# Kernel optimization log

Hardware: AMD Instinct MI355X
Metric: run time of the kernel (lower is better)

The kernel has to match this reference:

```python
import jax, jax.numpy as jnp
import numpy as np

CAP = 6.0
EPS = 1e-5

def _layernorm(x, g, b):
    mu = jnp.mean(x, axis=-1, keepdims=True)
    var = jnp.mean(jnp.square(x - mu), axis=-1, keepdims=True)
    return (x - mu) * jax.lax.rsqrt(var + EPS) * g + b

def setup_inputs() -> dict:
    key = jax.random.key(0)
    B, S, D, H = 4, 1024, 1024, 16
    DF = int(D * 2.0)
    ks = jax.random.split(key, 8)
    inp = {
        "x": jax.random.normal(ks[0], (B, S, D), dtype=jnp.float32),
        "mask": jnp.tril(jnp.ones((S, S), dtype=bool)),  # causal block mask
        "qkv_w": jax.random.normal(ks[1], (3 * D, D), dtype=jnp.float32) * 0.02,
        "qkv_b": jnp.zeros((3 * D,), dtype=jnp.float32),
        "out_w": jax.random.normal(ks[2], (D, D), dtype=jnp.float32) * 0.02,
        "out_b": jnp.zeros((D,), dtype=jnp.float32),
        "ln1_g": jnp.ones((D,), dtype=jnp.float32),
        "ln1_b": jnp.zeros((D,), dtype=jnp.float32),
        "ln2_g": jnp.ones((D,), dtype=jnp.float32),
        "ln2_b": jnp.zeros((D,), dtype=jnp.float32),
        "ff1_w": jax.random.normal(ks[3], (DF, D), dtype=jnp.float32) * 0.02,
        "ff1_b": jnp.zeros((DF,), dtype=jnp.float32),
        "ff2_w": jax.random.normal(ks[4], (D, DF), dtype=jnp.float32) * 0.02,
        "ff2_b": jnp.zeros((D,), dtype=jnp.float32),
    }
    return inp

def reference(x, mask, qkv_w, qkv_b, out_w, out_b, ln1_g, ln1_b, ln2_g, ln2_b,
              ff1_w, ff1_b, ff2_w, ff2_b):
    B, S, D = x.shape
    H = 16
    dh = D // H
    res = x
    h = _layernorm(x, ln1_g, ln1_b)
    qkv = h @ qkv_w.T + qkv_b                       # [B,S,3D]
    qkv = qkv.reshape(B, S, 3, H, dh).transpose(2, 0, 3, 1, 4)  # [3,B,H,S,dh]
    q, k, v = qkv[0], qkv[1], qkv[2]
    scores = jnp.einsum('bhqd,bhkd->bhqk', q, k) / jnp.sqrt(jnp.float32(dh))
    scores = CAP * jnp.tanh(scores / CAP)            # logit soft-cap score_mod
    scores = jnp.where(mask, scores, jnp.float32(-1e9))
    attn = jax.nn.softmax(scores, axis=-1)
    o = jnp.einsum('bhqk,bhkd->bhqd', attn, v)       # [B,H,S,dh]
    o = o.transpose(0, 2, 1, 3).reshape(B, S, D)
    x = res + (o @ out_w.T + out_b)
    h2 = _layernorm(x, ln2_g, ln2_b)
    ff = jax.nn.gelu(h2 @ ff1_w.T + ff1_b, approximate=False) @ ff2_w.T + ff2_b
    return x + ff
```

## Files before the change

kernel.cpp:

```cpp
#include <hip/hip_runtime.h>
#include <hip/hip_bf16.h>
#include <cmath>

#define NROWS 4096
#define DM    1024

typedef unsigned short u16;
typedef __attribute__((ext_vector_type(8))) short short8;
typedef __attribute__((ext_vector_type(4))) float floatx4;

#if __has_builtin(__builtin_amdgcn_exp2f)
#define EXP2F(x) __builtin_amdgcn_exp2f(x)
#else
#define EXP2F(x) exp2f(x)
#endif
#if __has_builtin(__builtin_amdgcn_rcpf)
#define RCPF(x) __builtin_amdgcn_rcpf(x)
#else
#define RCPF(x) (1.0f / (x))
#endif

__device__ __forceinline__ u16 f2bf(float f) {
    unsigned int u = __float_as_uint(f);
    return (u16)((u + 0x7fffu + ((u >> 16) & 1u)) >> 16);
}

__device__ __forceinline__ size_t pk_off(int row, int k, int KB) {
    const int rt = row >> 6, i = (row >> 4) & 3, lr = row & 15;
    const int kb = k >> 6, s = (k >> 5) & 1, lq = (k >> 3) & 3, j = k & 7;
    return ((((size_t)(rt * KB + kb) * 2 + s) * 4 + i) * 64 + lq * 16 + lr) * 8 + j;
}

__global__ __launch_bounds__(256) void castln_kernel(
    const float* __restrict__ s0, const float* __restrict__ s1,
    const float* __restrict__ s2, const float* __restrict__ s3,
    u16* __restrict__ d0, u16* __restrict__ d1,
    u16* __restrict__ d2, u16* __restrict__ d3,
    const float* __restrict__ x, const float* __restrict__ g,
    const float* __restrict__ beta, u16* __restrict__ hout)
{
    const int bid = blockIdx.x;
    if (bid < 8192) {
        const float* s; u16* d; int base, kbits, KB;
        if (bid < 3072)      { s = s0; d = d0; base = bid;        kbits = 10; KB = 16; }
        else if (bid < 4096) { s = s1; d = d1; base = bid - 3072; kbits = 10; KB = 16; }
        else if (bid < 6144) { s = s2; d = d2; base = bid - 4096; kbits = 10; KB = 16; }
        else                 { s = s3; d = d3; base = bid - 6144; kbits = 11; KB = 32; }
        const int idx = (base * 256 + threadIdx.x) * 4;
        const float4 v = *(const float4*)(s + idx);
        const int row = idx >> kbits, k = idx & ((1 << kbits) - 1);
        *(ushort4*)(d + pk_off(row, k, KB)) =
            make_ushort4(f2bf(v.x), f2bf(v.y), f2bf(v.z), f2bf(v.w));
        return;
    }
    const int row = bid - 8192;
    const int t = threadIdx.x;
    const float4 v = ((const float4*)(x + (size_t)row * DM))[t];
    float s = v.x + v.y + v.z + v.w;
    #pragma unroll
    for (int off = 32; off > 0; off >>= 1) s += __shfl_xor(s, off);
    __shared__ float red[4];
    const int wid = t >> 6;
    if ((t & 63) == 0) red[wid] = s;
    __syncthreads();
    const float mean = (red[0] + red[1] + red[2] + red[3]) * (1.0f / DM);
    const float dx = v.x - mean, dy = v.y - mean, dz = v.z - mean, dw = v.w - mean;
    float ss = dx*dx + dy*dy + dz*dz + dw*dw;
    #pragma unroll
    for (int off = 32; off > 0; off >>= 1) ss += __shfl_xor(ss, off);
    __syncthreads();
    if ((t & 63) == 0) red[wid] = ss;
    __syncthreads();
    const float var = (red[0] + red[1] + red[2] + red[3]) * (1.0f / DM);
    const float rstd = rsqrtf(var + 1e-5f);
    const float4 gv = ((const float4*)g)[t];
    const float4 bv = ((const float4*)beta)[t];
    *(ushort4*)(hout + pk_off(row, t * 4, 16)) = make_ushort4(
        f2bf(dx * rstd * gv.x + bv.x), f2bf(dy * rstd * gv.y + bv.y),
        f2bf(dz * rstd * gv.z + bv.z), f2bf(dw * rstd * gv.w + bv.w));
}

__global__ __launch_bounds__(256) void ln_kernel(
    const float* __restrict__ x, const float* __restrict__ g,
    const float* __restrict__ beta, u16* __restrict__ out)
{
    const int row = blockIdx.x;
    const int t = threadIdx.x;
    const float4 v = ((const float4*)(x + (size_t)row * DM))[t];
    float s = v.x + v.y + v.z + v.w;
    #pragma unroll
    for (int off = 32; off > 0; off >>= 1) s += __shfl_xor(s, off);
    __shared__ float red[4];
    const int wid = t >> 6;
    if ((t & 63) == 0) red[wid] = s;
    __syncthreads();
    const float mean = (red[0] + red[1] + red[2] + red[3]) * (1.0f / DM);
    const float dx = v.x - mean, dy = v.y - mean, dz = v.z - mean, dw = v.w - mean;
    float ss = dx*dx + dy*dy + dz*dz + dw*dw;
    #pragma unroll
    for (int off = 32; off > 0; off >>= 1) ss += __shfl_xor(ss, off);
    __syncthreads();
    if ((t & 63) == 0) red[wid] = ss;
    __syncthreads();
    const float var = (red[0] + red[1] + red[2] + red[3]) * (1.0f / DM);
    const float rstd = rsqrtf(var + 1e-5f);
    const float4 gv = ((const float4*)g)[t];
    const float4 bv = ((const float4*)beta)[t];
    *(ushort4*)(out + pk_off(row, t * 4, 16)) = make_ushort4(
        f2bf(dx * rstd * gv.x + bv.x), f2bf(dy * rstd * gv.y + bv.y),
        f2bf(dz * rstd * gv.z + bv.z), f2bf(dw * rstd * gv.w + bv.w));
}

__device__ __forceinline__ float gelu_f(float v) {
    return 0.5f * v * (1.0f + erff(v * 0.70710678118654752f));
}

template <int ACT, int OUTMODE, int TM>
__global__ __launch_bounds__(256, TM == 128 ? 3 : 4) void gemm_pk_kernel(
    const u16* __restrict__ A, const u16* __restrict__ W,
    const float* __restrict__ bias, const float* __restrict__ res,
    void* __restrict__ Cout, u16* __restrict__ vpout, u16* __restrict__ kpout,
    int N, int K)
{
    constexpr int MI = TM / 32;
    constexpr int SMEMB = (OUTMODE == 1) ? 34816 : 17408;
    __shared__ __align__(16) char smem[SMEMB];
    float* Cs = (float*)smem;

    const int tid = threadIdx.x;
    const int w = tid >> 6, l = tid & 63;
    const int lr = l & 15, lq = l >> 4;
    const int wm = w >> 1, wn = w & 1;

    const int fid = blockIdx.x;
    const int NB = (N >> 7) >> 3;
    const int xcd = fid & 7;
    const int kk = fid >> 3;
    constexpr int MT_BITS = (TM == 128) ? 5 : 6;
    constexpr int MT_MASK = (1 << MT_BITS) - 1;
    const int nt = xcd * NB + (kk >> MT_BITS);
    const int mt = kk & MT_MASK;
    const int m0 = mt * TM, n0 = nt * 128;
    const int KB = K >> 6;

    const int art = (TM == 128) ? (mt * 2 + wm) : mt;
    const u16* Ab = A + (size_t)art * KB * 4096 + l * 8;
    const u16* Wb = W + (size_t)(nt * 2 + wn) * KB * 4096 + l * 8;

    floatx4 acc[MI][4] = {};
    short8 a0[MI], b0[4], a1[MI], b1[4];
    #pragma unroll
    for (int i = 0; i < MI; i++) {
        const int fi = (TM == 128) ? i : (wm * 2 + i);
        a0[i] = *(const short8*)(Ab + fi * 512);
    }
    #pragma unroll
    for (int j = 0; j < 4; j++) b0[j] = *(const short8*)(Wb + j * 512);

    const int steps = K >> 5;
    for (int t = 0; t < steps; t += 2) {
        const u16* An = Ab + (size_t)(t + 1) * 2048;
        const u16* Wn = Wb + (size_t)(t + 1) * 2048;
        #pragma unroll
        for (int i = 0; i < MI; i++) {
            const int fi = (TM == 128) ? i : (wm * 2 + i);
            a1[i] = *(const short8*)(An + fi * 512);
        }
        #pragma unroll
        for (int j = 0; j < 4; j++) b1[j] = *(const short8*)(Wn + j * 512);
        #pragma unroll
        for (int i = 0; i < MI; i++)
            #pragma unroll
            for (int j = 0; j < 4; j++)
                acc[i][j] = __builtin_amdgcn_mfma_f32_16x16x32_bf16(a0[i], b0[j], acc[i][j], 0, 0, 0);
        if (t + 2 < steps) {
            const u16* An2 = Ab + (size_t)(t + 2) * 2048;
            const u16* Wn2 = Wb + (size_t)(t + 2) * 2048;
            #pragma unroll
            for (int i = 0; i < MI; i++) {
                const int fi = (TM == 128) ? i : (wm * 2 + i);
                a0[i] = *(const short8*)(An2 + fi * 512);
            }
            #pragma unroll
            for (int j = 0; j < 4; j++) b0[j] = *(const short8*)(Wn2 + j * 512);
        }
        #pragma unroll
        for (int i = 0; i < MI; i++)
            #pragma unroll
            for (int j = 0; j < 4; j++)
                acc[i][j] = __builtin_amdgcn_mfma_f32_16x16x32_bf16(a1[i], b1[j], acc[i][j], 0, 0, 0);
    }

    if (OUTMODE == 1) {
        short* Ts = (short*)smem;
        float bj[4];
        #pragma unroll
        for (int j = 0; j < 4; j++) bj[j] = bias[n0 + wn * 64 + j * 16 + lr];
        const bool isV = (n0 >= 2048);
        if (isV) {
            #pragma unroll
            for (int i = 0; i < 4; i++)
                #pragma unroll
                for (int j = 0; j < 4; j++) {
                    const int vcol_l = wn * 64 + j * 16 + lr;
                    const int sbase = wm * 64 + i * 16 + lq * 4;
                    #pragma unroll
                    for (int rp = 0; rp < 2; rp++) {
                        const unsigned pkv =
                            (unsigned)f2bf(acc[i][j][rp * 2] + bj[j]) |
                            ((unsigned)f2bf(acc[i][j][rp * 2 + 1] + bj[j]) << 16);
                        *(unsigned*)&Ts[vcol_l * 136 + sbase + rp * 2] = pkv;
                    }
                }
        } else {
            #pragma unroll
            for (int i = 0; i < 4; i++)
                #pragma unroll
                for (int j = 0; j < 4; j++)
                    #pragma unroll
                    for (int r = 0; r < 4; r++) {
                        const int row_l = wm * 64 + i * 16 + lq * 4 + r;
                        const int col_l = wn * 64 + j * 16 + lr;
                        Ts[row_l * 136 + col_l] = (short)f2bf(acc[i][j][r] + bj[j]);
                    }
        }
        __syncthreads();
        u16* dbuf = isV ? vpout : (n0 >= 1024 ? kpout : (u16*)Cout);
        const int hbase = (n0 & 1023) >> 6;
        const int l0 = (tid * 2) & 63, subp = tid >> 6, sp = (tid >> 5) & 1;
        #pragma unroll
        for (int tl = 0; tl < 2; tl++) {
            const int mg = m0 + tl * 64;
            const int bb2 = mg >> 10, ktile = (mg & 1023) >> 6;
            #pragma unroll
            for (int hl = 0; hl < 2; hl++) {
                const int hh = hbase + hl;
                u16* dst = dbuf + ((size_t)(bb2 * 16 + hh) * 16 + ktile) * 4096 + tid * 16;
                #pragma unroll
                for (int half = 0; half < 2; half++) {
                    const int ll = l0 + half;
                    short8 seg;
                    if (isV) {
                        const int vcol_l = hl * 64 + subp * 16 + (ll & 15);
                        const int srow = tl * 64 + sp * 32 + ((ll >> 4) & 3) * 8;
                        seg = *(const short8*)&Ts[vcol_l * 136 + srow];
                    } else {
                        const int row_l = tl * 64 + subp * 16 + (ll & 15);
                        const int col_l = hl * 64 + sp * 32 + ((ll >> 4) & 3) * 8;
                        seg = *(const short8*)&Ts[row_l * 136 + col_l];
                    }
                    *(short8*)(dst + half * 8) = seg;
                }
            }
        }
        return;
    }

    #pragma unroll
    for (int i = 0; i < MI; i++) {
        __syncthreads();
        #pragma unroll
        for (int r = 0; r < 4; r++) {
            const int rl = wm * 16 + lq * 4 + r;
            #pragma unroll
            for (int j = 0; j < 4; j++)
                Cs[rl * 136 + wn * 64 + j * 16 + lr] = acc[i][j][r];
        }
        __syncthreads();
        #pragma unroll
        for (int q = 0; q < 2; q++) {
            const int s2 = tid * 2 + q;
            const int rid = s2 >> 4, c8 = s2 & 15;
            const int rr = m0 + (rid >> 4) * (TM / 2) + i * 16 + (rid & 15);
            const int col = c8 * 8;
            float vv[8];
            const float4 v0 = *(const float4*)&Cs[rid * 136 + col];
            const float4 v1 = *(const float4*)&Cs[rid * 136 + col + 4];
            const float4 ba = *(const float4*)&bias[n0 + col];
            const float4 bb4 = *(const float4*)&bias[n0 + col + 4];
            vv[0] = v0.x + ba.x;  vv[1] = v0.y + ba.y;  vv[2] = v0.z + ba.z;  vv[3] = v0.w + ba.w;
            vv[4] = v1.x + bb4.x; vv[5] = v1.y + bb4.y; vv[6] = v1.z + bb4.z; vv[7] = v1.w + bb4.w;
            if (ACT) {
                #pragma unroll
                for (int e = 0; e < 8; e++) vv[e] = gelu_f(vv[e]);
            }
            if (OUTMODE == 0) {
                const size_t o0 = (size_t)rr * N + n0 + col;
                if (res) {
                    const float4 r0 = *(const float4*)&res[o0];
                    const float4 r1 = *(const float4*)&res[o0 + 4];
                    vv[0]+=r0.x; vv[1]+=r0.y; vv[2]+=r0.z; vv[3]+=r0.w;
                    vv[4]+=r1.x; vv[5]+=r1.y; vv[6]+=r1.z; vv[7]+=r1.w;
                }
                *(float4*)((float*)Cout + o0)     = make_float4(vv[0], vv[1], vv[2], vv[3]);
                *(float4*)((float*)Cout + o0 + 4) = make_float4(vv[4], vv[5], vv[6], vv[7]);
            } else {
                short8 ov;
                #pragma unroll
                for (int e = 0; e < 8; e++) ov[e] = (short)f2bf(vv[e]);
                *(short8*)((u16*)Cout + pk_off(rr, n0 + col, N >> 6)) = ov;
            }
        }
    }
}

__global__ __launch_bounds__(256, 3) void attn_mfma_kernel(
    const u16* __restrict__ qp, const u16* __restrict__ kp,
    const u16* __restrict__ vp, u16* __restrict__ o)
{
    __shared__ __align__(16) short Ps[4][1152];
    __shared__ __align__(16) short Os[4096];

    const int qt = 15 - blockIdx.y;
    const int bh = blockIdx.x;
    const int b = bh >> 4, h = bh & 15;
    const int tid = threadIdx.x;
    const int w = tid >> 6, l = tid & 63;
    const int C = l & 15, Qd = l >> 4;

    const float C1f = 0.0601122935f, C2f = -17.3123404907f;

    const size_t headoff = (size_t)(b * 16 + h) * 16 * 4096;
    const u16* qb = qp + headoff + (size_t)qt * 4096 + w * 1024 + l * 8;
    const u16* kb = kp + headoff + l * 8;
    const u16* vb = vp + headoff + l * 8;

    short8 qf[2];
    qf[0] = *(const short8*)qb;
    qf[1] = *(const short8*)(qb + 512);

    float l_i = 0.f;
    floatx4 oacc[4] = {};

    short8 kf[8];
    #pragma unroll
    for (int i = 0; i < 8; i++) kf[i] = *(const short8*)(kb + i * 512);

    for (int kt = 0; kt <= qt; kt++) {
        const u16* vv_ = vb + (size_t)kt * 4096;
        short8 vf[8];
        #pragma unroll
        for (int j = 0; j < 8; j++) vf[j] = *(const short8*)(vv_ + j * 512);

        floatx4 sacc[4] = {};
        #pragma unroll
        for (int mt = 0; mt < 4; mt++)
            #pragma unroll
            for (int s = 0; s < 2; s++)
                sacc[mt] = __builtin_amdgcn_mfma_f32_16x16x32_bf16(kf[mt * 2 + s], qf[s], sacc[mt], 0, 0, 0);

        if (kt < qt) {
            const u16* kn_ = kb + (size_t)(kt + 1) * 4096;
            #pragma unroll
            for (int i = 0; i < 8; i++) kf[i] = *(const short8*)(kn_ + i * 512);
        }

        float p[16];
        float rs = 0.f;
        const bool diag = (kt == qt);
        const int qrow = qt * 64 + w * 16 + C;
        #pragma unroll
        for (int mt = 0; mt < 4; mt++)
            #pragma unroll
            for (int r = 0; r < 4; r++) {
                const float e = EXP2F(sacc[mt][r] * C1f);
                float pv = EXP2F(C2f * RCPF(e + 1.0f));
                if (diag) {
                    const int krow = kt * 64 + mt * 16 + Qd * 4 + r;
                    if (krow > qrow) pv = 0.f;
                }
                p[mt * 4 + r] = pv;
                rs += pv;
            }
        rs += __shfl_xor(rs, 16);
        rs += __shfl_xor(rs, 32);
        l_i += rs;

        #pragma unroll
        for (int mt = 0; mt < 4; mt++)
            #pragma unroll
            for (int pr = 0; pr < 2; pr++) {
                union { __hip_bfloat162 b2; unsigned u; } cv;
                cv.b2 = __float22bfloat162_rn(
                    make_float2(p[mt * 4 + pr * 2], p[mt * 4 + pr * 2 + 1]));
                *(unsigned*)&Ps[w][C * 72 + mt * 16 + Qd * 4 + pr * 2] = cv.u;
            }
        short8 pf[2];
        pf[0] = *(const short8*)&Ps[w][C * 72 + Qd * 8];
        pf[1] = *(const short8*)&Ps[w][C * 72 + 32 + Qd * 8];

        #pragma unroll
        for (int dt = 0; dt < 4; dt++)
            #pragma unroll
            for (int s = 0; s < 2; s++)
                oacc[dt] = __builtin_amdgcn_mfma_f32_16x16x32_bf16(pf[s], vf[dt * 2 + s], oacc[dt], 0, 0, 0);
    }

    float linv[4];
    #pragma unroll
    for (int r = 0; r < 4; r++) linv[r] = RCPF(__shfl(l_i, Qd * 4 + r));
    #pragma unroll
    for (int dt = 0; dt < 4; dt++) {
        const int s = dt >> 1;
        const int lqp = (dt & 1) * 2 + (C >> 3);
        const int jj = C & 7;
        #pragma unroll
        for (int r = 0; r < 4; r++)
            Os[((s * 4 + w) * 64 + lqp * 16 + Qd * 4 + r) * 8 + jj] =
                (short)f2bf(oacc[dt][r] * linv[r]);
    }
    __syncthreads();
    u16* obase = o + (size_t)((b * 16 + qt) * 16 + h) * 4096 + tid * 16;
    *(short8*)obase       = *(const short8*)&Os[tid * 16];
    *(short8*)(obase + 8) = *(const short8*)&Os[tid * 16 + 8];
}

extern "C" void kernel_launch(void* const* d_in, const int* in_sizes, int n_in,
                              void* d_out, int out_size, void* d_ws, size_t ws_size,
                              hipStream_t stream)
{
    (void)in_sizes; (void)n_in; (void)out_size; (void)ws_size;
    const float* x     = (const float*)d_in[0];
    const float* qkv_w = (const float*)d_in[2];
    const float* qkv_b = (const float*)d_in[3];
    const float* out_w = (const float*)d_in[4];
    const float* out_b = (const float*)d_in[5];
    const float* ln1_g = (const float*)d_in[6];
    const float* ln1_b = (const float*)d_in[7];
    const float* ln2_g = (const float*)d_in[8];
    const float* ln2_b = (const float*)d_in[9];
    const float* ff1_w = (const float*)d_in[10];
    const float* ff1_b = (const float*)d_in[11];
    const float* ff2_w = (const float*)d_in[12];
    const float* ff2_b = (const float*)d_in[13];
    float* out = (float*)d_out;

    u16* qpbuf = (u16*)d_ws;
    u16* kpbuf = qpbuf + 4194304;
    u16* vpbuf = kpbuf + 4194304;
    u16* hbuf  = (u16*)((char*)d_ws + 33554432);
    u16* obuf  = (u16*)((char*)d_ws + 41943040);
    u16* wq    = (u16*)((char*)d_ws + 50331648);
    u16* wo = wq + 3145728;
    u16* w1 = wo + 1048576;
    u16* w2 = w1 + 2097152;
    u16* ff1buf = (u16*)d_ws;

    castln_kernel<<<12288, 256, 0, stream>>>(
        qkv_w, out_w, ff1_w, ff2_w, wq, wo, w1, w2, x, ln1_g, ln1_b, hbuf);
    gemm_pk_kernel<0,1,128><<<768, 256, 0, stream>>>(
        hbuf, wq, qkv_b, nullptr, qpbuf, vpbuf, kpbuf, 3072, 1024);
    attn_mfma_kernel<<<dim3(64, 16), 256, 0, stream>>>(qpbuf, kpbuf, vpbuf, obuf);
    gemm_pk_kernel<0,0,64><<<512, 256, 0, stream>>>(
        obuf, wo, out_b, x, out, nullptr, nullptr, 1024, 1024);
    ln_kernel<<<NROWS, 256, 0, stream>>>(out, ln2_g, ln2_b, hbuf);
    gemm_pk_kernel<1,2,128><<<512, 256, 0, stream>>>(
        hbuf, w1, ff1_b, nullptr, ff1buf, nullptr, nullptr, 2048, 1024);
    gemm_pk_kernel<0,0,64><<<512, 256, 0, stream>>>(
        ff1buf, w2, ff2_b, out, out, nullptr, nullptr, 1024, 2048);
}
```

Measured before the change: 295.2 us.

## Stage GEMM operand tiles through LDS with async global_load_lds double buffering

```diff
diff --git a/kernel.cpp b/kernel.cpp
--- a/kernel.cpp
+++ b/kernel.cpp
@@ -23,6 +23,12 @@
 __device__ __forceinline__ u16 f2bf(float f) {
     unsigned int u = __float_as_uint(f);
     return (u16)((u + 0x7fffu + ((u >> 16) & 1u)) >> 16);
+}
+
+__device__ __forceinline__ void gl_lds16(const u16* g, u16* l) {
+    __builtin_amdgcn_global_load_lds(
+        (const __attribute__((address_space(1))) unsigned int*)g,
+        (__attribute__((address_space(3))) unsigned int*)l, 16, 0, 0);
 }
 
 __device__ __forceinline__ size_t pk_off(int row, int k, int KB) {
@@ -116,15 +122,18 @@
 }
 
 template <int ACT, int OUTMODE, int TM>
-__global__ __launch_bounds__(256, TM == 128 ? 3 : 4) void gemm_pk_kernel(
+__global__ __launch_bounds__(256, 2) void gemm_pk_kernel(
     const u16* __restrict__ A, const u16* __restrict__ W,
     const float* __restrict__ bias, const float* __restrict__ res,
     void* __restrict__ Cout, u16* __restrict__ vpout, u16* __restrict__ kpout,
     int N, int K)
 {
     constexpr int MI = TM / 32;
-    constexpr int SMEMB = (OUTMODE == 1) ? 34816 : 17408;
+    constexpr int NCH = (TM == 128) ? 4 : 3;
+    constexpr int STAGE_U16 = NCH * 4096;
+    constexpr int SMEMB = 2 * STAGE_U16 * 2;
     __shared__ __align__(16) char smem[SMEMB];
+    u16* St = (u16*)smem;
     float* Cs = (float*)smem;
 
     const int tid = threadIdx.x;
@@ -143,52 +152,63 @@
     const int m0 = mt * TM, n0 = nt * 128;
     const int KB = K >> 6;
 
-    const int art = (TM == 128) ? (mt * 2 + wm) : mt;
-    const u16* Ab = A + (size_t)art * KB * 4096 + l * 8;
-    const u16* Wb = W + (size_t)(nt * 2 + wn) * KB * 4096 + l * 8;
+    const u16* gch[NCH];
+    if (TM == 128) {
+        gch[0] = A + (size_t)(mt * 2 + 0) * KB * 4096;
+        gch[1] = A + (size_t)(mt * 2 + 1) * KB * 4096;
+        gch[2] = W + (size_t)(nt * 2 + 0) * KB * 4096;
+        gch[3] = W + (size_t)(nt * 2 + 1) * KB * 4096;
+    } else {
+        gch[0] = A + (size_t)mt * KB * 4096;
+        gch[1] = W + (size_t)(nt * 2 + 0) * KB * 4096;
+        gch[2] = W + (size_t)(nt * 2 + 1) * KB * 4096;
+    }
 
     floatx4 acc[MI][4] = {};
-    short8 a0[MI], b0[4], a1[MI], b1[4];
-    #pragma unroll
-    for (int i = 0; i < MI; i++) {
-        const int fi = (TM == 128) ? i : (wm * 2 + i);
-        a0[i] = *(const short8*)(Ab + fi * 512);
-    }
-    #pragma unroll
-    for (int j = 0; j < 4; j++) b0[j] = *(const short8*)(Wb + j * 512);
-
-    const int steps = K >> 5;
-    for (int t = 0; t < steps; t += 2) {
-        const u16* An = Ab + (size_t)(t + 1) * 2048;
-        const u16* Wn = Wb + (size_t)(t + 1) * 2048;
-        #pragma unroll
-        for (int i = 0; i < MI; i++) {
-            const int fi = (TM == 128) ? i : (wm * 2 + i);
-            a1[i] = *(const short8*)(An + fi * 512);
-        }
-        #pragma unroll
-        for (int j = 0; j < 4; j++) b1[j] = *(const short8*)(Wn + j * 512);
-        #pragma unroll
-        for (int i = 0; i < MI; i++)
+
+    auto STAGE = [&](int kb, int buf) {
+        u16* dst = St + buf * STAGE_U16;
+        #pragma unroll
+        for (int c = 0; c < NCH; c++) {
+            const u16* src = gch[c] + (size_t)kb * 4096 + w * 512 + l * 8;
+            u16* ld = dst + c * 4096 + w * 512;
+            gl_lds16(src, ld);
+            gl_lds16(src + 2048, ld + 2048);
+        }
+    };
+
+    auto COMPUTE = [&](int buf) {
+        const u16* Sb = St + buf * STAGE_U16;
+        #pragma unroll
+        for (int ts = 0; ts < 2; ts++) {
+            short8 af[MI], bf[4];
+            #pragma unroll
+            for (int i = 0; i < MI; i++) {
+                const int off = (TM == 128) ? (wm * 4096 + ts * 2048 + i * 512)
+                                            : (ts * 2048 + (wm * 2 + i) * 512);
+                af[i] = *(const short8*)(Sb + off + l * 8);
+            }
+            constexpr int BB = (TM == 128) ? 2 : 1;
             #pragma unroll
             for (int j = 0; j < 4; j++)
-                acc[i][j] = __builtin_amdgcn_mfma_f32_16x16x32_bf16(a0[i], b0[j], acc[i][j], 0, 0, 0);
-        if (t + 2 < steps) {
-            const u16* An2 = Ab + (size_t)(t + 2) * 2048;
-            const u16* Wn2 = Wb + (size_t)(t + 2) * 2048;
-            #pragma unroll
-            for (int i = 0; i < MI; i++) {
-                const int fi = (TM == 128) ? i : (wm * 2 + i);
-                a0[i] = *(const short8*)(An2 + fi * 512);
-            }
-            #pragma unroll
-            for (int j = 0; j < 4; j++) b0[j] = *(const short8*)(Wn2 + j * 512);
-        }
-        #pragma unroll
-        for (int i = 0; i < MI; i++)
-            #pragma unroll
-            for (int j = 0; j < 4; j++)
-                acc[i][j] = __builtin_amdgcn_mfma_f32_16x16x32_bf16(a1[i], b1[j], acc[i][j], 0, 0, 0);
+                bf[j] = *(const short8*)(Sb + (BB + wn) * 4096 + ts * 2048 + j * 512 + l * 8);
+            #pragma unroll
+            for (int i = 0; i < MI; i++)
+                #pragma unroll
+                for (int j = 0; j < 4; j++)
+                    acc[i][j] = __builtin_amdgcn_mfma_f32_16x16x32_bf16(af[i], bf[j], acc[i][j], 0, 0, 0);
+        }
+    };
+
+    const int NKB = K >> 6;
+    STAGE(0, 0);
+    __syncthreads();
+    int cur = 0;
+    for (int kb = 0; kb < NKB; kb++) {
+        if (kb + 1 < NKB) STAGE(kb + 1, cur ^ 1);
+        COMPUTE(cur);
+        __syncthreads();
+        cur ^= 1;
     }
 
     if (OUTMODE == 1) {
```

Result: faster. 279.6 us (-5.3%).

## Use 64-row GEMM tiles everywhere with four-stage register prefetch pipeline

Applied to the files above, without the earlier changes.

```diff
diff --git a/kernel.cpp b/kernel.cpp
--- a/kernel.cpp
+++ b/kernel.cpp
@@ -115,15 +115,14 @@
     return 0.5f * v * (1.0f + erff(v * 0.70710678118654752f));
 }
 
-template <int ACT, int OUTMODE, int TM>
-__global__ __launch_bounds__(256, TM == 128 ? 3 : 4) void gemm_pk_kernel(
+template <int ACT, int OUTMODE>
+__global__ __launch_bounds__(256, 3) void gemm_pk_kernel(
     const u16* __restrict__ A, const u16* __restrict__ W,
     const float* __restrict__ bias, const float* __restrict__ res,
     void* __restrict__ Cout, u16* __restrict__ vpout, u16* __restrict__ kpout,
     int N, int K)
 {
-    constexpr int MI = TM / 32;
-    constexpr int SMEMB = (OUTMODE == 1) ? 34816 : 17408;
+    constexpr int SMEMB = (OUTMODE == 1) ? 18944 : 17408;
     __shared__ __align__(16) char smem[SMEMB];
     float* Cs = (float*)smem;
 
@@ -136,60 +135,49 @@
     const int NB = (N >> 7) >> 3;
     const int xcd = fid & 7;
     const int kk = fid >> 3;
-    constexpr int MT_BITS = (TM == 128) ? 5 : 6;
-    constexpr int MT_MASK = (1 << MT_BITS) - 1;
-    const int nt = xcd * NB + (kk >> MT_BITS);
-    const int mt = kk & MT_MASK;
-    const int m0 = mt * TM, n0 = nt * 128;
+    const int nt = xcd * NB + (kk >> 6);
+    const int mt = kk & 63;
+    const int m0 = mt * 64, n0 = nt * 128;
     const int KB = K >> 6;
 
-    const int art = (TM == 128) ? (mt * 2 + wm) : mt;
-    const u16* Ab = A + (size_t)art * KB * 4096 + l * 8;
+    const u16* Ab = A + (size_t)mt * KB * 4096 + l * 8;
     const u16* Wb = W + (size_t)(nt * 2 + wn) * KB * 4096 + l * 8;
 
-    floatx4 acc[MI][4] = {};
-    short8 a0[MI], b0[4], a1[MI], b1[4];
-    #pragma unroll
-    for (int i = 0; i < MI; i++) {
-        const int fi = (TM == 128) ? i : (wm * 2 + i);
-        a0[i] = *(const short8*)(Ab + fi * 512);
-    }
-    #pragma unroll
-    for (int j = 0; j < 4; j++) b0[j] = *(const short8*)(Wb + j * 512);
+    floatx4 acc[2][4] = {};
+    short8 As[4][2], Bs[4][4];
+
+#define LOADST(t, s) do {                                                    \
+    const u16* An_ = Ab + (size_t)(t) * 2048;                                \
+    const u16* Wn_ = Wb + (size_t)(t) * 2048;                                \
+    _Pragma("unroll")                                                        \
+    for (int i_ = 0; i_ < 2; i_++)                                           \
+        As[s][i_] = *(const short8*)(An_ + (wm * 2 + i_) * 512);             \
+    _Pragma("unroll")                                                        \
+    for (int j_ = 0; j_ < 4; j_++)                                           \
+        Bs[s][j_] = *(const short8*)(Wn_ + j_ * 512);                        \
+} while (0)
+
+#define MFMAS(s) do {                                                        \
+    _Pragma("unroll")                                                        \
+    for (int i_ = 0; i_ < 2; i_++)                                           \
+        _Pragma("unroll")                                                    \
+        for (int j_ = 0; j_ < 4; j_++)                                       \
+            acc[i_][j_] = __builtin_amdgcn_mfma_f32_16x16x32_bf16(           \
+                As[s][i_], Bs[s][j_], acc[i_][j_], 0, 0, 0);                 \
+} while (0)
 
     const int steps = K >> 5;
-    for (int t = 0; t < steps; t += 2) {
-        const u16* An = Ab + (size_t)(t + 1) * 2048;
-        const u16* Wn = Wb + (size_t)(t + 1) * 2048;
-        #pragma unroll
-        for (int i = 0; i < MI; i++) {
-            const int fi = (TM == 128) ? i : (wm * 2 + i);
-            a1[i] = *(const short8*)(An + fi * 512);
-        }
-        #pragma unroll
-        for (int j = 0; j < 4; j++) b1[j] = *(const short8*)(Wn + j * 512);
-        #pragma unroll
-        for (int i = 0; i < MI; i++)
-            #pragma unroll
-            for (int j = 0; j < 4; j++)
-                acc[i][j] = __builtin_amdgcn_mfma_f32_16x16x32_bf16(a0[i], b0[j], acc[i][j], 0, 0, 0);
-        if (t + 2 < steps) {
-            const u16* An2 = Ab + (size_t)(t + 2) * 2048;
-            const u16* Wn2 = Wb + (size_t)(t + 2) * 2048;
-            #pragma unroll
-            for (int i = 0; i < MI; i++) {
-                const int fi = (TM == 128) ? i : (wm * 2 + i);
-                a0[i] = *(const short8*)(An2 + fi * 512);
-            }
-            #pragma unroll
-            for (int j = 0; j < 4; j++) b0[j] = *(const short8*)(Wn2 + j * 512);
-        }
-        #pragma unroll
-        for (int i = 0; i < MI; i++)
-            #pragma unroll
-            for (int j = 0; j < 4; j++)
-                acc[i][j] = __builtin_amdgcn_mfma_f32_16x16x32_bf16(a1[i], b1[j], acc[i][j], 0, 0, 0);
-    }
+    LOADST(0, 0); LOADST(1, 1); LOADST(2, 2); LOADST(3, 3);
+    for (int t = 0; t + 4 < steps; t += 4) {
+        MFMAS(0); LOADST(t + 4, 0);
+        MFMAS(1); LOADST(t + 5, 1);
+        MFMAS(2); LOADST(t + 6, 2);
+        MFMAS(3); LOADST(t + 7, 3);
+    }
+    MFMAS(0); MFMAS(1); MFMAS(2); MFMAS(3);
+
+#undef LOADST
+#undef MFMAS
 
     if (OUTMODE == 1) {
         short* Ts = (short*)smem;
@@ -199,27 +187,27 @@
         const bool isV = (n0 >= 2048);
         if (isV) {
             #pragma unroll
-            for (int i = 0; i < 4; i++)
+            for (int i = 0; i < 2; i++)
                 #pragma unroll
                 for (int j = 0; j < 4; j++) {
                     const int vcol_l = wn * 64 + j * 16 + lr;
-                    const int sbase = wm * 64 + i * 16 + lq * 4;
+                    const int sbase = wm * 32 + i * 16 + lq * 4;
                     #pragma unroll
                     for (int rp = 0; rp < 2; rp++) {
                         const unsigned pkv =
                             (unsigned)f2bf(acc[i][j][rp * 2] + bj[j]) |
                             ((unsigned)f2bf(acc[i][j][rp * 2 + 1] + bj[j]) << 16);
-                        *(unsigned*)&Ts[vcol_l * 136 + sbase + rp * 2] = pkv;
+                        *(unsigned*)&Ts[vcol_l * 72 + sbase + rp * 2] = pkv;
                     }
                 }
         } else {
             #pragma unroll
-            for (int i = 0; i < 4; i++)
+            for (int i = 0; i < 2; i++)
                 #pragma unroll
                 for (int j = 0; j < 4; j++)
                     #pragma unroll
                     for (int r = 0; r < 4; r++) {
-                        const int row_l = wm * 64 + i * 16 + lq * 4 + r;
+                        const int row_l = wm * 32 + i * 16 + lq * 4 + r;
                         const int col_l = wn * 64 + j * 16 + lr;
                         Ts[row_l * 136 + col_l] = (short)f2bf(acc[i][j][r] + bj[j]);
                     }
@@ -228,36 +216,32 @@
         u16* dbuf = isV ? vpout : (n0 >= 1024 ? kpout : (u16*)Cout);
         const int hbase = (n0 & 1023) >> 6;
         const int l0 = (tid * 2) & 63, subp = tid >> 6, sp = (tid >> 5) & 1;
-        #pragma unroll
-        for (int tl = 0; tl < 2; tl++) {
-            const int mg = m0 + tl * 64;
-            const int bb2 = mg >> 10, ktile = (mg & 1023) >> 6;
-            #pragma unroll
-            for (int hl = 0; hl < 2; hl++) {
-                const int hh = hbase + hl;
-                u16* dst = dbuf + ((size_t)(bb2 * 16 + hh) * 16 + ktile) * 4096 + tid * 16;
-                #pragma unroll
-                for (int half = 0; half < 2; half++) {
-                    const int ll = l0 + half;
-                    short8 seg;
-                    if (isV) {
-                        const int vcol_l = hl * 64 + subp * 16 + (ll & 15);
-                        const int srow = tl * 64 + sp * 32 + ((ll >> 4) & 3) * 8;
-                        seg = *(const short8*)&Ts[vcol_l * 136 + srow];
-                    } else {
-                        const int row_l = tl * 64 + subp * 16 + (ll & 15);
-                        const int col_l = hl * 64 + sp * 32 + ((ll >> 4) & 3) * 8;
-                        seg = *(const short8*)&Ts[row_l * 136 + col_l];
-                    }
-                    *(short8*)(dst + half * 8) = seg;
+        const int bb2 = m0 >> 10, ktile = (m0 & 1023) >> 6;
+        #pragma unroll
+        for (int hl = 0; hl < 2; hl++) {
+            const int hh = hbase + hl;
+            u16* dst = dbuf + ((size_t)(bb2 * 16 + hh) * 16 + ktile) * 4096 + tid * 16;
+            #pragma unroll
+            for (int half = 0; half < 2; half++) {
+                const int ll = l0 + half;
+                short8 seg;
+                if (isV) {
+                    const int vcol_l = hl * 64 + subp * 16 + (ll & 15);
+                    const int srow = sp * 32 + ((ll >> 4) & 3) * 8;
+                    seg = *(const short8*)&Ts[vcol_l * 72 + srow];
+                } else {
+                    const int row_l = subp * 16 + (ll & 15);
+                    const int col_l = hl * 64 + sp * 32 + ((ll >> 4) & 3) * 8;
+                    seg = *(const short8*)&Ts[row_l * 136 + col_l];
                 }
+                *(short8*)(dst + half * 8) = seg;
             }
         }
         return;
     }
 
     #pragma unroll
-    for (int i = 0; i < MI; i++) {
+    for (int i = 0; i < 2; i++) {
         __syncthreads();
         #pragma unroll
         for (int r = 0; r < 4; r++) {
@@ -271,7 +255,7 @@
         for (int q = 0; q < 2; q++) {
             const int s2 = tid * 2 + q;
             const int rid = s2 >> 4, c8 = s2 & 15;
-            const int rr = m0 + (rid >> 4) * (TM / 2) + i * 16 + (rid & 15);
+            const int rr = m0 + (rid >> 4) * 32 + i * 16 + (rid & 15);
             const int col = c8 * 8;
             float vv[8];
             const float4 v0 = *(const float4*)&Cs[rid * 136 + col];
@@ -448,14 +432,14 @@
 
     castln_kernel<<<12288, 256, 0, stream>>>(
         qkv_w, out_w, ff1_w, ff2_w, wq, wo, w1, w2, x, ln1_g, ln1_b, hbuf);
-    gemm_pk_kernel<0,1,128><<<768, 256, 0, stream>>>(
+    gemm_pk_kernel<0,1><<<1536, 256, 0, stream>>>(
         hbuf, wq, qkv_b, nullptr, qpbuf, vpbuf, kpbuf, 3072, 1024);
     attn_mfma_kernel<<<dim3(64, 16), 256, 0, stream>>>(qpbuf, kpbuf, vpbuf, obuf);
-    gemm_pk_kernel<0,0,64><<<512, 256, 0, stream>>>(
+    gemm_pk_kernel<0,0><<<512, 256, 0, stream>>>(
         obuf, wo, out_b, x, out, nullptr, nullptr, 1024, 1024);
     ln_kernel<<<NROWS, 256, 0, stream>>>(out, ln2_g, ln2_b, hbuf);
-    gemm_pk_kernel<1,2,128><<<512, 256, 0, stream>>>(
+    gemm_pk_kernel<1,2><<<1024, 256, 0, stream>>>(
         hbuf, w1, ff1_b, nullptr, ff1buf, nullptr, nullptr, 2048, 1024);
-    gemm_pk_kernel<0,0,64><<<512, 256, 0, stream>>>(
+    gemm_pk_kernel<0,0><<<512, 256, 0, stream>>>(
         ff1buf, w2, ff2_b, out, out, nullptr, nullptr, 1024, 2048);
 }
```

Result: slower. 306.4 us (+3.8%).
